# Kernel tuning notes

Hardware: AMD Instinct MI355X
Metric: run time of the kernel (lower is better)

Reference implementation:

```python
import jax, jax.numpy as jnp
import numpy as np

D_MODEL = 512

def setup_inputs() -> dict:
    key = jax.random.key(0)
    k1, k2, k3 = jax.random.split(key, 3)
    B, N1, N2 = 16, 2048, 2048
    x1 = jax.random.normal(k1, (B, N1, D_MODEL), dtype=jnp.float32)
    x2 = jax.random.normal(k2, (B, N2, D_MODEL), dtype=jnp.float32)
    node_mask = jnp.ones((B, N1), dtype=jnp.bool_)
    # learned parameter: q_proj weight, stored torch-style [out, in]
    Wq = jax.random.normal(k3, (D_MODEL, D_MODEL), dtype=jnp.float32) * (1.0 / np.sqrt(D_MODEL))
    return {"x1": x1, "x2": x2, "node_mask": node_mask, "Wq": Wq}


def reference(x1, x2, node_mask, Wq):
    # Q = x1 @ Wq^T   (torch Linear with weight [out, in], no bias)
    Q = jnp.einsum('bnd,ed->bne', x1, Wq)            # [B, N1, 512]
    D = x2                                            # [B, N2, 512]
    # similarity matrix L = Q @ D^T
    L = jnp.einsum('bnd,bmd->bnm', Q, D)              # [B, N1, N2]
    # attention over document axis (dim=2)
    A_D = jax.nn.softmax(L, axis=2)                   # [B, N1, N2]
    # C_D = Q^T @ A_D -> transposed to [B, N2, 512]
    C_D = jnp.einsum('bnd,bnm->bmd', Q, A_D)          # [B, N2, 512]
    # attention over query axis (dim=1), then transposed: A_Q [B, N2, N1]
    A_Q = jnp.swapaxes(jax.nn.softmax(L, axis=1), 1, 2)
    # C_Q = D^T @ A_Q -> transposed to [B, N1, 512]
    C_Q = jnp.einsum('bmd,bmn->bnd', D, A_Q)          # [B, N1, 512]
    return (C_Q, C_D, A_D, A_Q)
```

## Files before the change

kernel.cpp:

```cpp
#include <hip/hip_runtime.h>

namespace {

constexpr int Bn = 16;
constexpr int Nn = 2048;
constexpr int Dn = 512;

typedef _Float16 h4 __attribute__((ext_vector_type(4)));
typedef _Float16 h8 __attribute__((ext_vector_type(8)));
typedef float    fx4 __attribute__((ext_vector_type(4)));

__device__ __forceinline__ void gld16(const _Float16* g, _Float16* l) {
  typedef const void __attribute__((address_space(1))) gvoid;
  typedef void __attribute__((address_space(3))) lvoid;
  __builtin_amdgcn_global_load_lds((gvoid*)g, (lvoid*)l, 16, 0, 0);
}

__device__ __forceinline__ void stage_gld(const _Float16* __restrict__ g, int ld,
    int r0, int k0, _Float16* __restrict__ lds, int t)
{
  #pragma unroll
  for (int i = 0; i < 2; ++i) {
    int chunk = i*256 + t;
    gld16(g + (long)(r0 + (chunk >> 2))*ld + k0 + (chunk & 3)*8, lds + chunk*8);
  }
}

__device__ __forceinline__ void load_f32(const float* __restrict__ g, int ld,
    int r0, int k0, int t, fx4* regs)
{
  #pragma unroll
  for (int rd = 0; rd < 4; ++rd)
    regs[rd] = *(const fx4*)(g + (long)(r0 + rd*32 + (t >> 3))*ld + k0 + (t & 7)*4);
}

template<int MODE, int S>
__device__ __forceinline__ void write_f16(const fx4* regs, _Float16* __restrict__ lds,
    int t, int k0, const float* __restrict__ km, const float* __restrict__ ki)
{
  const int c = (t & 7)*4;
  fx4 vm, vi;
  if constexpr (MODE == 2) { vm = *(const fx4*)(km + k0 + c); vi = *(const fx4*)(ki + k0 + c); }
  #pragma unroll
  for (int rd = 0; rd < 4; ++rd) {
    int r = rd*32 + (t >> 3);
    h4 o;
    #pragma unroll
    for (int i = 0; i < 4; ++i) {
      if constexpr (MODE == 2) o[i] = (_Float16)(__expf(regs[rd][i] - vm[i]) * vi[i]);
      else                     o[i] = (_Float16)regs[rd][i];
    }
    *(h4*)(lds + r*S + c) = o;
  }
}

template<int MA, int MB, int EPI>
__global__ __launch_bounds__(256) void gemm128(
    const void* __restrict__ Ap, long sA,
    const void* __restrict__ Bp, long sB,
    void* __restrict__ Cp, long sC, int ldc,
    void* __restrict__ C2p, long sC2, int ldc2,
    int lda, int ldb, int K,
    const float* __restrict__ kmax, const float* __restrict__ kinv,
    float* __restrict__ rowPM, float* __restrict__ rowPS,
    float* __restrict__ colPM, float* __restrict__ colPS)
{
  constexpr int SA = (MA == 0) ? 32 : 40;
  constexpr int SB = (MB == 0) ? 32 : 40;
  constexpr int ASZ = 128*SA, BSZ = 128*SB;
  constexpr int DB = 2*ASZ + 2*BSZ;
  constexpr int SMEM = (EPI == 2 && DB < 128*136) ? 128*136 : DB;
  __shared__ _Float16 smem[SMEM];

  const int b = blockIdx.z;
  const int bx = blockIdx.x, by = blockIdx.y;
  const int row0 = bx*128, col0 = by*128;
  const int t = threadIdx.x, w = t >> 6, l = t & 63;
  const int wr = w >> 1, wc = w & 1, l15 = l & 15, lg = l >> 4;

  const void* Ab;
  const void* Bb;
  if constexpr (MA == 0) Ab = (const void*)((const _Float16*)Ap + (long)b*sA);
  else                   Ab = (const void*)((const float*)Ap + (long)b*sA);
  if constexpr (MB == 0) Bb = (const void*)((const _Float16*)Bp + (long)b*sB);
  else                   Bb = (const void*)((const float*)Bp + (long)b*sB);

  const float* km = nullptr; const float* ki = nullptr;
  if constexpr (MA == 2) { km = kmax + (long)b*Nn; ki = kinv + (long)b*Nn; }

  fx4 acc[4][4];
  #pragma unroll
  for (int fi = 0; fi < 4; ++fi)
    #pragma unroll
    for (int fj = 0; fj < 4; ++fj)
      acc[fi][fj] = (fx4){0.f, 0.f, 0.f, 0.f};

  const int NT = K/32;
  fx4 regA[4], regB[4];

  if constexpr (MA == 0) stage_gld((const _Float16*)Ab, lda, row0, 0, smem, t);
  else                   load_f32((const float*)Ab, lda, row0, 0, t, regA);
  if constexpr (MB == 0) stage_gld((const _Float16*)Bb, ldb, col0, 0, smem + 2*ASZ, t);
  else                   load_f32((const float*)Bb, ldb, col0, 0, t, regB);
  if constexpr (MA != 0) write_f16<MA, SA>(regA, smem, t, 0, km, ki);
  if constexpr (MB != 0) write_f16<1, SB>(regB, smem + 2*ASZ, t, 0, nullptr, nullptr);
  __syncthreads();

  for (int kt = 0; kt < NT; ++kt) {
    const int cur = kt & 1, nxt = cur ^ 1;
    const int k1 = (kt + 1)*32;
    _Float16* cA = smem + cur*ASZ;
    _Float16* cB = smem + 2*ASZ + cur*BSZ;
    _Float16* nA = smem + nxt*ASZ;
    _Float16* nB = smem + 2*ASZ + nxt*BSZ;

    if (kt + 1 < NT) {
      if constexpr (MA == 0) stage_gld((const _Float16*)Ab, lda, row0, k1, nA, t);
      else                   load_f32((const float*)Ab, lda, row0, k1, t, regA);
      if constexpr (MB == 0) stage_gld((const _Float16*)Bb, ldb, col0, k1, nB, t);
      else                   load_f32((const float*)Bb, ldb, col0, k1, t, regB);
    }

    h8 af[4], bf[4];
    #pragma unroll
    for (int fi = 0; fi < 4; ++fi)
      af[fi] = *(const h8*)(cA + (wr*64 + fi*16 + l15)*SA + lg*8);
    #pragma unroll
    for (int fj = 0; fj < 4; ++fj)
      bf[fj] = *(const h8*)(cB + (wc*64 + fj*16 + l15)*SB + lg*8);
    #pragma unroll
    for (int fi = 0; fi < 4; ++fi)
      #pragma unroll
      for (int fj = 0; fj < 4; ++fj)
        acc[fi][fj] = __builtin_amdgcn_mfma_f32_16x16x32_f16(af[fi], bf[fj], acc[fi][fj], 0, 0, 0);

    if (kt + 1 < NT) {
      if constexpr (MA != 0) write_f16<MA, SA>(regA, nA, t, k1, km, ki);
      if constexpr (MB != 0) write_f16<1, SB>(regB, nB, t, k1, nullptr, nullptr);
    }
    __syncthreads();
  }

  if constexpr (EPI <= 1) {
    float* Cb = (float*)Cp + (long)b*sC;
    #pragma unroll
    for (int fi = 0; fi < 4; ++fi)
      #pragma unroll
      for (int fj = 0; fj < 4; ++fj)
        #pragma unroll
        for (int j = 0; j < 4; ++j)
          Cb[(long)(row0 + wr*64 + fi*16 + lg*4 + j)*ldc + col0 + wc*64 + fj*16 + l15] = acc[fi][fj][j];
  }

  if constexpr (EPI == 1) {
    float rm[4][4], rs[4][4];
    #pragma unroll
    for (int fi = 0; fi < 4; ++fi)
      #pragma unroll
      for (int j = 0; j < 4; ++j)
        rm[fi][j] = fmaxf(fmaxf(acc[fi][0][j], acc[fi][1][j]),
                          fmaxf(acc[fi][2][j], acc[fi][3][j]));
    #pragma unroll
    for (int m = 1; m < 16; m <<= 1)
      #pragma unroll
      for (int fi = 0; fi < 4; ++fi)
        #pragma unroll
        for (int j = 0; j < 4; ++j)
          rm[fi][j] = fmaxf(rm[fi][j], __shfl_xor(rm[fi][j], m, 64));
    #pragma unroll
    for (int fi = 0; fi < 4; ++fi)
      #pragma unroll
      for (int j = 0; j < 4; ++j) {
        float s = 0.f;
        #pragma unroll
        for (int fj = 0; fj < 4; ++fj)
          s += __expf(acc[fi][fj][j] - rm[fi][j]);
        rs[fi][j] = s;
      }
    #pragma unroll
    for (int m = 1; m < 16; m <<= 1)
      #pragma unroll
      for (int fi = 0; fi < 4; ++fi)
        #pragma unroll
        for (int j = 0; j < 4; ++j)
          rs[fi][j] += __shfl_xor(rs[fi][j], m, 64);
    if (l15 == 0) {
      #pragma unroll
      for (int fi = 0; fi < 4; ++fi)
        #pragma unroll
        for (int j = 0; j < 4; ++j) {
          int row = row0 + wr*64 + fi*16 + lg*4 + j;
          long idx = ((long)b*Nn + row)*32 + by*2 + wc;
          rowPM[idx] = rm[fi][j];
          rowPS[idx] = rs[fi][j];
        }
    }
    float cm[4], cs[4];
    #pragma unroll
    for (int fj = 0; fj < 4; ++fj) {
      float v = -3.4e38f;
      #pragma unroll
      for (int fi = 0; fi < 4; ++fi)
        #pragma unroll
        for (int j = 0; j < 4; ++j)
          v = fmaxf(v, acc[fi][fj][j]);
      cm[fj] = v;
    }
    #pragma unroll
    for (int fj = 0; fj < 4; ++fj) {
      cm[fj] = fmaxf(cm[fj], __shfl_xor(cm[fj], 16, 64));
      cm[fj] = fmaxf(cm[fj], __shfl_xor(cm[fj], 32, 64));
    }
    #pragma unroll
    for (int fj = 0; fj < 4; ++fj) {
      float s = 0.f;
      #pragma unroll
      for (int fi = 0; fi < 4; ++fi)
        #pragma unroll
        for (int j = 0; j < 4; ++j)
          s += __expf(acc[fi][fj][j] - cm[fj]);
      cs[fj] = s;
    }
    #pragma unroll
    for (int fj = 0; fj < 4; ++fj) {
      cs[fj] += __shfl_xor(cs[fj], 16, 64);
      cs[fj] += __shfl_xor(cs[fj], 32, 64);
    }
    if (l < 16) {
      #pragma unroll
      for (int fj = 0; fj < 4; ++fj) {
        int col = col0 + wc*64 + fj*16 + l15;
        long idx = ((long)b*Nn + col)*32 + bx*2 + wr;
        colPM[idx] = cm[fj];
        colPS[idx] = cs[fj];
      }
    }
  }

  if constexpr (EPI == 2) {
    #pragma unroll
    for (int fi = 0; fi < 4; ++fi)
      #pragma unroll
      for (int fj = 0; fj < 4; ++fj)
        #pragma unroll
        for (int j = 0; j < 4; ++j)
          smem[(wr*64 + fi*16 + lg*4 + j)*136 + wc*64 + fj*16 + l15] = (_Float16)acc[fi][fj][j];
    __syncthreads();
    _Float16* Qb  = (_Float16*)Cp  + (long)b*sC;
    _Float16* QTb = (_Float16*)C2p + (long)b*sC2;
    #pragma unroll
    for (int rd = 0; rd < 8; ++rd) {
      int r = rd*16 + (t >> 4), c8 = (t & 15)*8;
      h8 v = *(const h8*)(smem + r*136 + c8);
      *(h8*)(Qb + (long)(row0 + r)*ldc + col0 + c8) = v;
    }
    #pragma unroll
    for (int rd = 0; rd < 8; ++rd) {
      int dl = rd*16 + (t >> 4), n8 = (t & 15)*8;
      h8 v;
      #pragma unroll
      for (int i = 0; i < 8; ++i) v[i] = smem[(n8 + i)*136 + dl];
      *(h8*)(QTb + (long)(col0 + dl)*ldc2 + row0 + n8) = v;
    }
  }
}

__global__ __launch_bounds__(256) void convert_x2(const float* __restrict__ x2,
    _Float16* __restrict__ x2h, _Float16* __restrict__ x2hT)
{
  __shared__ _Float16 lt[64*66];
  const int b = blockIdx.z, m0 = blockIdx.x*64, d0 = blockIdx.y*64;
  const int t = threadIdx.x;
  const float* xb = x2 + (long)b*Nn*Dn;
  _Float16* hb = x2h + (long)b*Nn*Dn;
  #pragma unroll
  for (int rd = 0; rd < 4; ++rd) {
    int r = rd*16 + (t >> 4), c = (t & 15)*4;
    fx4 v = *(const fx4*)(xb + (long)(m0 + r)*Dn + d0 + c);
    h4 h;
    #pragma unroll
    for (int i = 0; i < 4; ++i) { h[i] = (_Float16)v[i]; lt[r*66 + c + i] = h[i]; }
    *(h4*)(hb + (long)(m0 + r)*Dn + d0 + c) = h;
  }
  __syncthreads();
  _Float16* tb = x2hT + (long)b*Dn*Nn;
  #pragma unroll
  for (int rd = 0; rd < 4; ++rd) {
    int dl = rd*16 + (t >> 4), ml = (t & 15)*4;
    h4 h;
    #pragma unroll
    for (int i = 0; i < 4; ++i) h[i] = lt[(ml + i)*66 + dl];
    *(h4*)(tb + (long)(d0 + dl)*Nn + m0 + ml) = h;
  }
}

__global__ __launch_bounds__(256) void reduce_stats(
    const float* __restrict__ rowPM, const float* __restrict__ rowPS,
    const float* __restrict__ colPM, const float* __restrict__ colPS,
    float* __restrict__ rmaxF, float* __restrict__ rinv,
    float* __restrict__ cmaxF, float* __restrict__ cinv)
{
  const int w = threadIdx.x >> 6, l = threadIdx.x & 63;
  const long row = (long)blockIdx.x*4 + w;
  const float* PM = blockIdx.y ? colPM : rowPM;
  const float* PS = blockIdx.y ? colPS : rowPS;
  float m0 = PM[row*32 + (l & 31)];
  float s0 = PS[row*32 + (l & 31)];
  float m = m0;
  #pragma unroll
  for (int k = 1; k < 32; k <<= 1) m = fmaxf(m, __shfl_xor(m, k, 64));
  float v = s0 * __expf(m0 - m);
  #pragma unroll
  for (int k = 1; k < 32; k <<= 1) v += __shfl_xor(v, k, 64);
  if (l == 0) {
    if (blockIdx.y == 0) { rmaxF[row] = m; rinv[row] = 1.f / v; }
    else                 { cmaxF[row] = m; cinv[row] = 1.f / v; }
  }
}

__global__ __launch_bounds__(256) void finalize(float* __restrict__ AD, float* __restrict__ AQ,
    _Float16* __restrict__ At,
    const float* __restrict__ rmaxF, const float* __restrict__ rinv,
    const float* __restrict__ cmaxF, const float* __restrict__ cinv)
{
  __shared__ float l2[64*65];
  __shared__ _Float16 l1[64*66];
  const int b = blockIdx.z, n0 = blockIdx.x*64, m0 = blockIdx.y*64;
  const int t = threadIdx.x;
  float* Lb = AD + (long)b*Nn*Nn;
  #pragma unroll
  for (int rd = 0; rd < 4; ++rd) {
    int r = rd*16 + (t >> 4), c = (t & 15)*4;
    long off = (long)(n0 + r)*Nn + m0 + c;
    fx4 v = *(const fx4*)(Lb + off);
    float rm = rmaxF[(long)b*Nn + n0 + r];
    float ri = rinv [(long)b*Nn + n0 + r];
    fx4 cm = *(const fx4*)(cmaxF + (long)b*Nn + m0 + c);
    fx4 ci = *(const fx4*)(cinv  + (long)b*Nn + m0 + c);
    fx4 e1;
    #pragma unroll
    for (int i = 0; i < 4; ++i) {
      e1[i] = __expf(v[i] - rm) * ri;
      float e2 = __expf(v[i] - cm[i]) * ci[i];
      l2[r*65 + c + i] = e2;
      l1[r*66 + c + i] = (_Float16)e1[i];
    }
    *(fx4*)(Lb + off) = e1;
  }
  __syncthreads();
  float* Qb = AQ + (long)b*Nn*Nn;
  _Float16* Atb = At + (long)b*Nn*Nn;
  #pragma unroll
  for (int rd = 0; rd < 4; ++rd) {
    int ml = rd*16 + (t >> 4), nl = (t & 15)*4;
    fx4 q; h4 h;
    #pragma unroll
    for (int i = 0; i < 4; ++i) { q[i] = l2[(nl + i)*65 + ml]; h[i] = l1[(nl + i)*66 + ml]; }
    *(fx4*)(Qb + (long)(m0 + ml)*Nn + n0 + nl) = q;
    *(h4*)(Atb + (long)(m0 + ml)*Nn + n0 + nl) = h;
  }
}

}

extern "C" void kernel_launch(void* const* d_in, const int* in_sizes, int n_in,
                              void* d_out, int out_size, void* d_ws, size_t ws_size,
                              hipStream_t stream)
{
  const float* x1 = (const float*)d_in[0];
  const float* x2 = (const float*)d_in[1];
  const float* Wq = (const float*)d_in[3];

  float* out = (float*)d_out;
  float* C_Q = out;
  float* C_D = out + (long)Bn*Nn*Dn;
  float* A_D = out + 2L*Bn*Nn*Dn;
  float* A_Q = A_D + (long)Bn*Nn*Nn;

  char* ws = (char*)d_ws;
  _Float16* Qh   = (_Float16*)ws;
  _Float16* QhT  = Qh   + (long)Bn*Nn*Dn;
  _Float16* x2h  = QhT  + (long)Bn*Dn*Nn;
  _Float16* x2hT = x2h  + (long)Bn*Nn*Dn;
  _Float16* At   = x2hT + (long)Bn*Dn*Nn;
  float* rowPM = (float*)At;
  float* rowPS = rowPM + (long)Bn*Nn*32;
  float* colPM = rowPS + (long)Bn*Nn*32;
  float* colPS = colPM + (long)Bn*Nn*32;
  float* rmaxF = (float*)(At + (long)Bn*Nn*Nn);
  float* rinv  = rmaxF + (long)Bn*Nn;
  float* cmaxF = rinv  + (long)Bn*Nn;
  float* cinv  = cmaxF + (long)Bn*Nn;

  dim3 blk(256);

  convert_x2<<<dim3(32, 8, 16), blk, 0, stream>>>(x2, x2h, x2hT);

  gemm128<1,1,2><<<dim3(16, 4, 16), blk, 0, stream>>>(
      x1, (long)Nn*Dn, Wq, 0L,
      Qh, (long)Nn*Dn, Dn, QhT, (long)Dn*Nn, Nn,
      Dn, Dn, Dn,
      nullptr, nullptr, nullptr, nullptr, nullptr, nullptr);

  gemm128<0,0,1><<<dim3(16, 16, 16), blk, 0, stream>>>(
      Qh, (long)Nn*Dn, x2h, (long)Nn*Dn,
      A_D, (long)Nn*Nn, Nn, nullptr, 0L, 0,
      Dn, Dn, Dn,
      nullptr, nullptr, rowPM, rowPS, colPM, colPS);

  reduce_stats<<<dim3(Bn*Nn/4, 2), blk, 0, stream>>>(rowPM, rowPS, colPM, colPS,
                                                     rmaxF, rinv, cmaxF, cinv);

  gemm128<2,0,0><<<dim3(16, 4, 16), blk, 0, stream>>>(
      A_D, (long)Nn*Nn, x2hT, (long)Dn*Nn,
      C_Q, (long)Nn*Dn, Dn, nullptr, 0L, 0,
      Nn, Nn, Nn,
      cmaxF, cinv, nullptr, nullptr, nullptr, nullptr);

  finalize<<<dim3(32, 32, 16), blk, 0, stream>>>(A_D, A_Q, At, rmaxF, rinv, cmaxF, cinv);

  gemm128<0,0,0><<<dim3(16, 4, 16), blk, 0, stream>>>(
      At, (long)Nn*Nn, QhT, (long)Dn*Nn,
      C_D, (long)Nn*Dn, Dn, nullptr, 0L, 0,
      Nn, Nn, Nn,
      nullptr, nullptr, nullptr, nullptr, nullptr, nullptr);
}
```

Measured before the change: 726.3 us.

## Store logits in fp16 workspace, fold softmax into log-offset, remap grid per XCD

The similarity GEMM now writes fp16 logits to a workspace instead of fp32 into A_D. Reduce_stats emits a single log-sum-exp offset per row or column. The C_Q GEMM reads the fp16 logits and applies exp(L - offset) on load. Finalize is split into an At-producing kernel and a final pass that writes both fp32 outputs, and the partial-stat and At scratch buffers are placed inside the A_Q output region. GEMM grids are flattened with an XCD-aware mapping that keeps each batch on specific XCDs for L2 locality. The aim is to cut HBM traffic from the large fp32 logit round-trips, at the cost of fp16 rounding of the logits before exp.

```diff
diff --git a/kernel.cpp b/kernel.cpp
--- a/kernel.cpp
+++ b/kernel.cpp
@@ -33,35 +33,70 @@
   for (int rd = 0; rd < 4; ++rd)
     regs[rd] = *(const fx4*)(g + (long)(r0 + rd*32 + (t >> 3))*ld + k0 + (t & 7)*4);
 }
-
-template<int MODE, int S>
-__device__ __forceinline__ void write_f16(const fx4* regs, _Float16* __restrict__ lds,
-    int t, int k0, const float* __restrict__ km, const float* __restrict__ ki)
+template<int S>
+__device__ __forceinline__ void write_cvt(const fx4* regs, _Float16* __restrict__ lds, int t)
 {
   const int c = (t & 7)*4;
-  fx4 vm, vi;
-  if constexpr (MODE == 2) { vm = *(const fx4*)(km + k0 + c); vi = *(const fx4*)(ki + k0 + c); }
   #pragma unroll
   for (int rd = 0; rd < 4; ++rd) {
     int r = rd*32 + (t >> 3);
     h4 o;
     #pragma unroll
-    for (int i = 0; i < 4; ++i) {
-      if constexpr (MODE == 2) o[i] = (_Float16)(__expf(regs[rd][i] - vm[i]) * vi[i]);
-      else                     o[i] = (_Float16)regs[rd][i];
-    }
+    for (int i = 0; i < 4; ++i) o[i] = (_Float16)regs[rd][i];
     *(h4*)(lds + r*S + c) = o;
   }
 }
 
-template<int MA, int MB, int EPI>
+struct RegsA3 { h8 v0, v1; fx4 k00, k01, k10, k11; };
+__device__ __forceinline__ void load_A3(const _Float16* __restrict__ g, int ld,
+    int r0, int k0, int t, const float* __restrict__ kofs, RegsA3& R)
+{
+  {
+    int chunk = t, r = chunk >> 2, c = (chunk & 3)*8;
+    R.v0  = *(const h8*)(g + (long)(r0 + r)*ld + k0 + c);
+    R.k00 = *(const fx4*)(kofs + k0 + c);
+    R.k01 = *(const fx4*)(kofs + k0 + c + 4);
+  }
+  {
+    int chunk = 256 + t, r = chunk >> 2, c = (chunk & 3)*8;
+    R.v1  = *(const h8*)(g + (long)(r0 + r)*ld + k0 + c);
+    R.k10 = *(const fx4*)(kofs + k0 + c);
+    R.k11 = *(const fx4*)(kofs + k0 + c + 4);
+  }
+}
+template<int S>
+__device__ __forceinline__ void write_A3(const RegsA3& R, _Float16* __restrict__ lds, int t)
+{
+  {
+    int chunk = t, r = chunk >> 2, c = (chunk & 3)*8;
+    h8 o;
+    #pragma unroll
+    for (int j = 0; j < 4; ++j) {
+      o[j]   = (_Float16)__expf((float)R.v0[j]   - R.k00[j]);
+      o[4+j] = (_Float16)__expf((float)R.v0[4+j] - R.k01[j]);
+    }
+    *(h8*)(lds + r*S + c) = o;
+  }
+  {
+    int chunk = 256 + t, r = chunk >> 2, c = (chunk & 3)*8;
+    h8 o;
+    #pragma unroll
+    for (int j = 0; j < 4; ++j) {
+      o[j]   = (_Float16)__expf((float)R.v1[j]   - R.k10[j]);
+      o[4+j] = (_Float16)__expf((float)R.v1[4+j] - R.k11[j]);
+    }
+    *(h8*)(lds + r*S + c) = o;
+  }
+}
+
+template<int MA, int MB, int EPI, int TY>
 __global__ __launch_bounds__(256) void gemm128(
     const void* __restrict__ Ap, long sA,
     const void* __restrict__ Bp, long sB,
     void* __restrict__ Cp, long sC, int ldc,
     void* __restrict__ C2p, long sC2, int ldc2,
     int lda, int ldb, int K,
-    const float* __restrict__ kmax, const float* __restrict__ kinv,
+    const float* __restrict__ kofs,
     float* __restrict__ rowPM, float* __restrict__ rowPS,
     float* __restrict__ colPM, float* __restrict__ colPS)
 {
@@ -69,24 +104,29 @@
   constexpr int SB = (MB == 0) ? 32 : 40;
   constexpr int ASZ = 128*SA, BSZ = 128*SB;
   constexpr int DB = 2*ASZ + 2*BSZ;
-  constexpr int SMEM = (EPI == 2 && DB < 128*136) ? 128*136 : DB;
+  constexpr int SMEM = (EPI >= 1 && DB < 128*136) ? 128*136 : DB;
   __shared__ _Float16 smem[SMEM];
 
-  const int b = blockIdx.z;
-  const int bx = blockIdx.x, by = blockIdx.y;
+  constexpr int TILES = 16*TY;
+  const int bid = blockIdx.x;
+  const int xcd = bid & 7, slot = bid >> 3;
+  const int b = xcd*2 + slot/TILES;
+  const int tile = slot % TILES;
+  const int by = tile % TY, bx = tile / TY;
   const int row0 = bx*128, col0 = by*128;
+
   const int t = threadIdx.x, w = t >> 6, l = t & 63;
   const int wr = w >> 1, wc = w & 1, l15 = l & 15, lg = l >> 4;
 
   const void* Ab;
   const void* Bb;
-  if constexpr (MA == 0) Ab = (const void*)((const _Float16*)Ap + (long)b*sA);
-  else                   Ab = (const void*)((const float*)Ap + (long)b*sA);
-  if constexpr (MB == 0) Bb = (const void*)((const _Float16*)Bp + (long)b*sB);
-  else                   Bb = (const void*)((const float*)Bp + (long)b*sB);
-
-  const float* km = nullptr; const float* ki = nullptr;
-  if constexpr (MA == 2) { km = kmax + (long)b*Nn; ki = kinv + (long)b*Nn; }
+  if constexpr (MA == 1) Ab = (const void*)((const float*)Ap + (long)b*sA);
+  else                   Ab = (const void*)((const _Float16*)Ap + (long)b*sA);
+  if constexpr (MB == 1) Bb = (const void*)((const float*)Bp + (long)b*sB);
+  else                   Bb = (const void*)((const _Float16*)Bp + (long)b*sB);
+
+  const float* ko = nullptr;
+  if constexpr (MA == 3) ko = kofs + (long)b*Nn;
 
   fx4 acc[4][4];
   #pragma unroll
@@ -97,13 +137,16 @@
 
   const int NT = K/32;
   fx4 regA[4], regB[4];
-
-  if constexpr (MA == 0) stage_gld((const _Float16*)Ab, lda, row0, 0, smem, t);
-  else                   load_f32((const float*)Ab, lda, row0, 0, t, regA);
-  if constexpr (MB == 0) stage_gld((const _Float16*)Bb, ldb, col0, 0, smem + 2*ASZ, t);
-  else                   load_f32((const float*)Bb, ldb, col0, 0, t, regB);
-  if constexpr (MA != 0) write_f16<MA, SA>(regA, smem, t, 0, km, ki);
-  if constexpr (MB != 0) write_f16<1, SB>(regB, smem + 2*ASZ, t, 0, nullptr, nullptr);
+  RegsA3 rA3;
+
+  if constexpr (MA == 0)      stage_gld((const _Float16*)Ab, lda, row0, 0, smem, t);
+  else if constexpr (MA == 1) load_f32((const float*)Ab, lda, row0, 0, t, regA);
+  else                        load_A3((const _Float16*)Ab, lda, row0, 0, t, ko, rA3);
+  if constexpr (MB == 0)      stage_gld((const _Float16*)Bb, ldb, col0, 0, smem + 2*ASZ, t);
+  else                        load_f32((const float*)Bb, ldb, col0, 0, t, regB);
+  if constexpr (MA == 1)      write_cvt<SA>(regA, smem, t);
+  if constexpr (MA == 3)      write_A3<SA>(rA3, smem, t);
+  if constexpr (MB == 1)      write_cvt<SB>(regB, smem + 2*ASZ, t);
   __syncthreads();
 
   for (int kt = 0; kt < NT; ++kt) {
@@ -115,10 +158,11 @@
     _Float16* nB = smem + 2*ASZ + nxt*BSZ;
 
     if (kt + 1 < NT) {
-      if constexpr (MA == 0) stage_gld((const _Float16*)Ab, lda, row0, k1, nA, t);
-      else                   load_f32((const float*)Ab, lda, row0, k1, t, regA);
-      if constexpr (MB == 0) stage_gld((const _Float16*)Bb, ldb, col0, k1, nB, t);
-      else                   load_f32((const float*)Bb, ldb, col0, k1, t, regB);
+      if constexpr (MA == 0)      stage_gld((const _Float16*)Ab, lda, row0, k1, nA, t);
+      else if constexpr (MA == 1) load_f32((const float*)Ab, lda, row0, k1, t, regA);
+      else                        load_A3((const _Float16*)Ab, lda, row0, k1, t, ko, rA3);
+      if constexpr (MB == 0)      stage_gld((const _Float16*)Bb, ldb, col0, k1, nB, t);
+      else                        load_f32((const float*)Bb, ldb, col0, k1, t, regB);
     }
 
     h8 af[4], bf[4];
@@ -135,13 +179,14 @@
         acc[fi][fj] = __builtin_amdgcn_mfma_f32_16x16x32_f16(af[fi], bf[fj], acc[fi][fj], 0, 0, 0);
 
     if (kt + 1 < NT) {
-      if constexpr (MA != 0) write_f16<MA, SA>(regA, nA, t, k1, km, ki);
-      if constexpr (MB != 0) write_f16<1, SB>(regB, nB, t, k1, nullptr, nullptr);
+      if constexpr (MA == 1) write_cvt<SA>(regA, nA, t);
+      if constexpr (MA == 3) write_A3<SA>(rA3, nA, t);
+      if constexpr (MB == 1) write_cvt<SB>(regB, nB, t);
     }
     __syncthreads();
   }
 
-  if constexpr (EPI <= 1) {
+  if constexpr (EPI == 0) {
     float* Cb = (float*)Cp + (long)b*sC;
     #pragma unroll
     for (int fi = 0; fi < 4; ++fi)
@@ -153,6 +198,30 @@
   }
 
   if constexpr (EPI == 1) {
+    #pragma unroll
+    for (int fi = 0; fi < 4; ++fi)
+      #pragma unroll
+      for (int fj = 0; fj < 4; ++fj)
+        #pragma unroll
+        for (int j = 0; j < 4; ++j)
+          acc[fi][fj][j] = (float)(_Float16)acc[fi][fj][j];
+
+    #pragma unroll
+    for (int fi = 0; fi < 4; ++fi)
+      #pragma unroll
+      for (int fj = 0; fj < 4; ++fj)
+        #pragma unroll
+        for (int j = 0; j < 4; ++j)
+          smem[(wr*64 + fi*16 + lg*4 + j)*136 + wc*64 + fj*16 + l15] = (_Float16)acc[fi][fj][j];
+    __syncthreads();
+    _Float16* Cb = (_Float16*)Cp + (long)b*sC;
+    #pragma unroll
+    for (int rd = 0; rd < 8; ++rd) {
+      int r = rd*16 + (t >> 4), c8 = (t & 15)*8;
+      h8 v = *(const h8*)(smem + r*136 + c8);
+      *(h8*)(Cb + (long)(row0 + r)*ldc + col0 + c8) = v;
+    }
+
     float rm[4][4], rs[4][4];
     #pragma unroll
     for (int fi = 0; fi < 4; ++fi)
@@ -297,8 +366,7 @@
 __global__ __launch_bounds__(256) void reduce_stats(
     const float* __restrict__ rowPM, const float* __restrict__ rowPS,
     const float* __restrict__ colPM, const float* __restrict__ colPS,
-    float* __restrict__ rmaxF, float* __restrict__ rinv,
-    float* __restrict__ cmaxF, float* __restrict__ cinv)
+    float* __restrict__ rofs, float* __restrict__ cofs)
 {
   const int w = threadIdx.x >> 6, l = threadIdx.x & 63;
   const long row = (long)blockIdx.x*4 + w;
@@ -313,51 +381,73 @@
   #pragma unroll
   for (int k = 1; k < 32; k <<= 1) v += __shfl_xor(v, k, 64);
   if (l == 0) {
-    if (blockIdx.y == 0) { rmaxF[row] = m; rinv[row] = 1.f / v; }
-    else                 { cmaxF[row] = m; cinv[row] = 1.f / v; }
-  }
-}
-
-__global__ __launch_bounds__(256) void finalize(float* __restrict__ AD, float* __restrict__ AQ,
-    _Float16* __restrict__ At,
-    const float* __restrict__ rmaxF, const float* __restrict__ rinv,
-    const float* __restrict__ cmaxF, const float* __restrict__ cinv)
-{
-  __shared__ float l2[64*65];
+    float ofs = m + __logf(v);
+    if (blockIdx.y == 0) rofs[row] = ofs;
+    else                 cofs[row] = ofs;
+  }
+}
+
+__global__ __launch_bounds__(256) void finalize_At(const _Float16* __restrict__ Lh,
+    _Float16* __restrict__ At, const float* __restrict__ rofs)
+{
   __shared__ _Float16 l1[64*66];
   const int b = blockIdx.z, n0 = blockIdx.x*64, m0 = blockIdx.y*64;
   const int t = threadIdx.x;
-  float* Lb = AD + (long)b*Nn*Nn;
+  const _Float16* Lb = Lh + (long)b*Nn*Nn;
   #pragma unroll
   for (int rd = 0; rd < 4; ++rd) {
     int r = rd*16 + (t >> 4), c = (t & 15)*4;
-    long off = (long)(n0 + r)*Nn + m0 + c;
-    fx4 v = *(const fx4*)(Lb + off);
-    float rm = rmaxF[(long)b*Nn + n0 + r];
-    float ri = rinv [(long)b*Nn + n0 + r];
-    fx4 cm = *(const fx4*)(cmaxF + (long)b*Nn + m0 + c);
-    fx4 ci = *(const fx4*)(cinv  + (long)b*Nn + m0 + c);
+    h4 v = *(const h4*)(Lb + (long)(n0 + r)*Nn + m0 + c);
+    float ro = rofs[(long)b*Nn + n0 + r];
+    #pragma unroll
+    for (int i = 0; i < 4; ++i)
+      l1[r*66 + c + i] = (_Float16)__expf((float)v[i] - ro);
+  }
+  __syncthreads();
+  _Float16* Ab = At + (long)b*Nn*Nn;
+  #pragma unroll
+  for (int rd = 0; rd < 4; ++rd) {
+    int ml = rd*16 + (t >> 4), nl = (t & 15)*4;
+    h4 h;
+    #pragma unroll
+    for (int i = 0; i < 4; ++i) h[i] = l1[(nl + i)*66 + ml];
+    *(h4*)(Ab + (long)(m0 + ml)*Nn + n0 + nl) = h;
+  }
+}
+
+__global__ __launch_bounds__(256) void finalize_AQ(const _Float16* __restrict__ Lh,
+    float* __restrict__ AD, float* __restrict__ AQ,
+    const float* __restrict__ rofs, const float* __restrict__ cofs)
+{
+  __shared__ float l2[64*65];
+  const int b = blockIdx.z, n0 = blockIdx.x*64, m0 = blockIdx.y*64;
+  const int t = threadIdx.x;
+  const _Float16* Lb = Lh + (long)b*Nn*Nn;
+  float* Db = AD + (long)b*Nn*Nn;
+  #pragma unroll
+  for (int rd = 0; rd < 4; ++rd) {
+    int r = rd*16 + (t >> 4), c = (t & 15)*4;
+    h4 v = *(const h4*)(Lb + (long)(n0 + r)*Nn + m0 + c);
+    float ro = rofs[(long)b*Nn + n0 + r];
+    fx4 co = *(const fx4*)(cofs + (long)b*Nn + m0 + c);
     fx4 e1;
     #pragma unroll
     for (int i = 0; i < 4; ++i) {
-      e1[i] = __expf(v[i] - rm) * ri;
-      float e2 = __expf(v[i] - cm[i]) * ci[i];
-      l2[r*65 + c + i] = e2;
-      l1[r*66 + c + i] = (_Float16)e1[i];
-    }
-    *(fx4*)(Lb + off) = e1;
+      float lv = (float)v[i];
+      e1[i] = __expf(lv - ro);
+      l2[r*65 + c + i] = __expf(lv - co[i]);
+    }
+    *(fx4*)(Db + (long)(n0 + r)*Nn + m0 + c) = e1;
   }
   __syncthreads();
   float* Qb = AQ + (long)b*Nn*Nn;
-  _Float16* Atb = At + (long)b*Nn*Nn;
   #pragma unroll
   for (int rd = 0; rd < 4; ++rd) {
     int ml = rd*16 + (t >> 4), nl = (t & 15)*4;
-    fx4 q; h4 h;
-    #pragma unroll
-    for (int i = 0; i < 4; ++i) { q[i] = l2[(nl + i)*65 + ml]; h[i] = l1[(nl + i)*66 + ml]; }
+    fx4 q;
+    #pragma unroll
+    for (int i = 0; i < 4; ++i) q[i] = l2[(nl + i)*65 + ml];
     *(fx4*)(Qb + (long)(m0 + ml)*Nn + n0 + nl) = q;
-    *(h4*)(Atb + (long)(m0 + ml)*Nn + n0 + nl) = h;
   }
 }
 
@@ -382,46 +472,47 @@
   _Float16* QhT  = Qh   + (long)Bn*Nn*Dn;
   _Float16* x2h  = QhT  + (long)Bn*Dn*Nn;
   _Float16* x2hT = x2h  + (long)Bn*Nn*Dn;
-  _Float16* At   = x2hT + (long)Bn*Dn*Nn;
-  float* rowPM = (float*)At;
+  _Float16* Lh   = x2hT + (long)Bn*Dn*Nn;
+  float* rofs = (float*)(Lh + (long)Bn*Nn*Nn);
+  float* cofs = rofs + (long)Bn*Nn;
+
+  float* rowPM = (float*)A_Q;
   float* rowPS = rowPM + (long)Bn*Nn*32;
   float* colPM = rowPS + (long)Bn*Nn*32;
   float* colPS = colPM + (long)Bn*Nn*32;
-  float* rmaxF = (float*)(At + (long)Bn*Nn*Nn);
-  float* rinv  = rmaxF + (long)Bn*Nn;
-  float* cmaxF = rinv  + (long)Bn*Nn;
-  float* cinv  = cmaxF + (long)Bn*Nn;
+  _Float16* At = (_Float16*)A_Q;
 
   dim3 blk(256);
 
   convert_x2<<<dim3(32, 8, 16), blk, 0, stream>>>(x2, x2h, x2hT);
 
-  gemm128<1,1,2><<<dim3(16, 4, 16), blk, 0, stream>>>(
+  gemm128<1,1,2,4><<<dim3(1024), blk, 0, stream>>>(
       x1, (long)Nn*Dn, Wq, 0L,
       Qh, (long)Nn*Dn, Dn, QhT, (long)Dn*Nn, Nn,
       Dn, Dn, Dn,
-      nullptr, nullptr, nullptr, nullptr, nullptr, nullptr);
-
-  gemm128<0,0,1><<<dim3(16, 16, 16), blk, 0, stream>>>(
+      nullptr, nullptr, nullptr, nullptr, nullptr);
+
+  gemm128<0,0,1,16><<<dim3(4096), blk, 0, stream>>>(
       Qh, (long)Nn*Dn, x2h, (long)Nn*Dn,
-      A_D, (long)Nn*Nn, Nn, nullptr, 0L, 0,
+      Lh, (long)Nn*Nn, Nn, nullptr, 0L, 0,
       Dn, Dn, Dn,
-      nullptr, nullptr, rowPM, rowPS, colPM, colPS);
-
-  reduce_stats<<<dim3(Bn*Nn/4, 2), blk, 0, stream>>>(rowPM, rowPS, colPM, colPS,
-                                                     rmaxF, rinv, cmaxF, cinv);
-
-  gemm128<2,0,0><<<dim3(16, 4, 16), blk, 0, stream>>>(
-      A_D, (long)Nn*Nn, x2hT, (long)Dn*Nn,
+      nullptr, rowPM, rowPS, colPM, colPS);
+
+  reduce_stats<<<dim3(Bn*Nn/4, 2), blk, 0, stream>>>(rowPM, rowPS, colPM, colPS, rofs, cofs);
+
+  gemm128<3,0,0,4><<<dim3(1024), blk, 0, stream>>>(
+      Lh, (long)Nn*Nn, x2hT, (long)Dn*Nn,
       C_Q, (long)Nn*Dn, Dn, nullptr, 0L, 0,
       Nn, Nn, Nn,
-      cmaxF, cinv, nullptr, nullptr, nullptr, nullptr);
-
-  finalize<<<dim3(32, 32, 16), blk, 0, stream>>>(A_D, A_Q, At, rmaxF, rinv, cmaxF, cinv);
-
-  gemm128<0,0,0><<<dim3(16, 4, 16), blk, 0, stream>>>(
+      cofs, nullptr, nullptr, nullptr, nullptr);
+
+  finalize_At<<<dim3(32, 32, 16), blk, 0, stream>>>(Lh, At, rofs);
+
+  gemm128<0,0,0,4><<<dim3(1024), blk, 0, stream>>>(
       At, (long)Nn*Nn, QhT, (long)Dn*Nn,
       C_D, (long)Nn*Dn, Dn, nullptr, 0L, 0,
       Nn, Nn, Nn,
-      nullptr, nullptr, nullptr, nullptr, nullptr, nullptr);
-}
+      nullptr, nullptr, nullptr, nullptr, nullptr);
+
+  finalize_AQ<<<dim3(32, 32, 16), blk, 0, stream>>>(Lh, A_D, A_Q, rofs, cofs);
+}
```

Result: faster. 624.1 us (-14.1%).
